# Optimization experiments

Measured on AMD Instinct MI355X. Metric: run time of the kernel, lower is better.

The kernel has to match this reference:

```python
import jax, jax.numpy as jnp
import numpy as np

N_NODES = 50000
N_EDGES = 800000
N_RELS = 200
D = 128


def setup_inputs() -> dict:
    key = jax.random.key(0)
    ks = jax.random.split(key, 9)
    h = jax.random.normal(ks[0], (N_NODES, D), dtype=jnp.float32)
    r = jax.random.normal(ks[1], (N_RELS, D), dtype=jnp.float32)
    norm = jax.random.uniform(ks[2], (N_NODES, 1), dtype=jnp.float32)
    src = jax.random.randint(ks[3], (N_EDGES,), 0, N_NODES, dtype=jnp.int32)
    dst = jax.random.randint(ks[4], (N_EDGES,), 0, N_NODES, dtype=jnp.int32)
    rel = jax.random.randint(ks[5], (N_EDGES,), 0, N_RELS, dtype=jnp.int32)
    stdv = 1.0 / np.sqrt(D)
    W_msg = jax.random.uniform(ks[6], (D, D), minval=-stdv, maxval=stdv, dtype=jnp.float32)
    W = jax.random.uniform(ks[7], (D, D), minval=-stdv, maxval=stdv, dtype=jnp.float32)
    b = jax.random.uniform(ks[8], (D,), minval=-stdv, maxval=stdv, dtype=jnp.float32)
    return {"h": h, "r": r, "norm": norm, "src": src, "dst": dst, "rel": rel,
            "W_msg": W_msg, "W": W, "b": b}


def reference(h, r, norm, src, dst, rel, W_msg, W, b):
    # dropout=0.0 (eval); h = h * norm (symmetric-norm pre-scale)
    hn = h * norm                                    # [N, D]
    # per-edge message: (h_src - r_rel) @ W_msg
    msg = (hn[src] - r[rel]) @ W_msg                 # [E, D]
    # scatter-sum to destination nodes, then post-scale by norm
    agg = jax.ops.segment_sum(msg, dst, num_segments=hn.shape[0]) * norm  # [N, D]
    out = hn @ W + agg + b
    return jax.nn.relu(out)
```

## Files before the change

### kernel.cpp

```cpp
#include <hip/hip_runtime.h>

#define N_NODES 50000
#define N_EDGES 800000
#define DIM 128
#define K2 256
#define NREL 200
#define BN2 128
#define NB2 391
#define ECAP 4096
#define EPB 4096

typedef unsigned short u16;
typedef __attribute__((ext_vector_type(8))) short short8;
typedef __attribute__((ext_vector_type(4))) float f32x4;

__device__ __forceinline__ float bf2f(u16 v) {
    union { unsigned int u; float f; } x;
    x.u = ((unsigned int)v) << 16;
    return x.f;
}

__device__ __forceinline__ u16 f2bf(float f) {
    union { unsigned int u; float f; } x;
    x.f = f;
    return (u16)((x.u + 0x7FFFu + ((x.u >> 16) & 1u)) >> 16);
}

__device__ __forceinline__ int sniff_fp32(const void* h, int tid) {
    const u16* hp = (const u16*)h;
    u16 v = hp[2 * (tid & 63)];
    float a = fabsf(bf2f(v));
    int insane = ((v & 0x7F80) == 0x7F80) || (a != 0.0f && (a > 1e6f || a < 1e-20f));
    return __popcll(__ballot(insane)) > 16;
}

#define PREP_H (N_NODES * 32)
#define PREP_R (NREL * 32)
#define PREP_W 8192
#define PREP_N (N_NODES / 4)
#define PREP_B 32
#define PREP_TOT (PREP_H + PREP_R + PREP_W + PREP_N + PREP_B)
#define PREP_BLOCKS ((PREP_TOT + 255) / 256)
#define HIST_BLOCKS 128
__global__ __launch_bounds__(256) void prep_hist(
    const void* __restrict__ h, const void* __restrict__ r, const void* __restrict__ norm,
    const void* __restrict__ W, const void* __restrict__ Wmsg, const void* __restrict__ bias,
    const int* __restrict__ dst,
    u16* __restrict__ hx, u16* __restrict__ r_bf, u16* __restrict__ wt,
    u16* __restrict__ norm_bf, float* __restrict__ b_f, int* __restrict__ bucketCount)
{
    __shared__ int hh[NB2];
    int tid = threadIdx.x;
    if (blockIdx.x >= PREP_BLOCKS) {
        for (int i = tid; i < NB2; i += 256) hh[i] = 0;
        __syncthreads();
        int stride = HIST_BLOCKS * 256;
        for (int e = (blockIdx.x - PREP_BLOCKS) * 256 + tid; e < N_EDGES; e += stride)
            atomicAdd(&hh[dst[e] >> 7], 1);
        __syncthreads();
        for (int i = tid; i < NB2; i += 256)
            if (hh[i]) atomicAdd(&bucketCount[i], hh[i]);
        return;
    }
    int isf = sniff_fp32(h, tid);
    int t = blockIdx.x * 256 + tid;
    if (t < PREP_H) {
        int n = t >> 5, c = t & 31;
        float4 v; float nv;
        if (isf) {
            nv = ((const float*)norm)[n];
            v = *(const float4*)((const float*)h + (size_t)n * DIM + c * 4);
        } else {
            nv = bf2f(((const u16*)norm)[n]);
            ushort4 u = *(const ushort4*)((const u16*)h + (size_t)n * DIM + c * 4);
            v = make_float4(bf2f(u.x), bf2f(u.y), bf2f(u.z), bf2f(u.w));
        }
        ushort4 o;
        o.x = f2bf(v.x * nv); o.y = f2bf(v.y * nv); o.z = f2bf(v.z * nv); o.w = f2bf(v.w * nv);
        *(ushort4*)(hx + (size_t)n * DIM + c * 4) = o;
    } else if (t < PREP_H + PREP_R) {
        int t2 = t - PREP_H;
        int rho = t2 >> 5, c = t2 & 31;
        float4 v;
        if (isf) v = *(const float4*)((const float*)r + (size_t)rho * DIM + c * 4);
        else {
            ushort4 u = *(const ushort4*)((const u16*)r + (size_t)rho * DIM + c * 4);
            v = make_float4(bf2f(u.x), bf2f(u.y), bf2f(u.z), bf2f(u.w));
        }
        ushort4 o;
        o.x = f2bf(v.x); o.y = f2bf(v.y); o.z = f2bf(v.z); o.w = f2bf(v.w);
        *(ushort4*)(r_bf + (size_t)rho * DIM + c * 4) = o;
    } else if (t < PREP_H + PREP_R + PREP_W) {
        int t3 = t - PREP_H - PREP_R;
        int j = t3 >> 6;
        int k0 = (t3 & 63) * 4;
        ushort4 o;
        u16* op = (u16*)&o;
        for (int kk = 0; kk < 4; ++kk) {
            int k = k0 + kk;
            float wv;
            if (isf) wv = (k < 128) ? ((const float*)W)[(size_t)k * DIM + j]
                                    : ((const float*)Wmsg)[(size_t)(k - 128) * DIM + j];
            else     wv = (k < 128) ? bf2f(((const u16*)W)[(size_t)k * DIM + j])
                                    : bf2f(((const u16*)Wmsg)[(size_t)(k - 128) * DIM + j]);
            op[kk] = f2bf(wv);
        }
        *(ushort4*)(wt + (size_t)j * K2 + k0) = o;
    } else if (t < PREP_H + PREP_R + PREP_W + PREP_N) {
        int n0 = (t - PREP_H - PREP_R - PREP_W) * 4;
        ushort4 o;
        if (isf) {
            float4 v = *(const float4*)((const float*)norm + n0);
            o.x = f2bf(v.x); o.y = f2bf(v.y); o.z = f2bf(v.z); o.w = f2bf(v.w);
        } else {
            o = *(const ushort4*)((const u16*)norm + n0);
        }
        *(ushort4*)(norm_bf + n0) = o;
    } else if (t < PREP_TOT) {
        int j0 = (t - PREP_H - PREP_R - PREP_W - PREP_N) * 4;
        float4 v;
        if (isf) v = *(const float4*)((const float*)bias + j0);
        else {
            ushort4 u = *(const ushort4*)((const u16*)bias + j0);
            v = make_float4(bf2f(u.x), bf2f(u.y), bf2f(u.z), bf2f(u.w));
        }
        *(float4*)(b_f + j0) = v;
    }
}

__global__ __launch_bounds__(512) void bucket_scan(const int* __restrict__ bucketCount,
                            int* __restrict__ bucketBase, int* __restrict__ bucketCursor) {
    __shared__ int sd[512];
    int t = threadIdx.x;
    int c = (t < NB2) ? bucketCount[t] : 0;
    sd[t] = c;
    __syncthreads();
    for (int off = 1; off < 512; off <<= 1) {
        int v = (t >= off) ? sd[t - off] : 0;
        __syncthreads();
        sd[t] += v;
        __syncthreads();
    }
    if (t < NB2) { int ex = sd[t] - c; bucketBase[t] = ex; bucketCursor[t] = ex; }
    if (t == 0) bucketBase[NB2] = N_EDGES;
}

__global__ __launch_bounds__(512) void fill_lds(
    const int* __restrict__ dst, const int* __restrict__ src, const int* __restrict__ rel,
    int* __restrict__ bucketCursor, int* __restrict__ spk)
{
    __shared__ int hist[NB2];
    __shared__ int lbase[NB2];
    __shared__ int gbase[NB2];
    __shared__ int sd[512];
    __shared__ int pay[EPB];
    __shared__ u16 bkt[EPB];
    int tid = threadIdx.x;
    for (int i = tid; i < NB2; i += 512) hist[i] = 0;
    __syncthreads();
    int e0 = blockIdx.x * EPB;
    int myb[8], myr[8], myp[8];
#pragma unroll
    for (int i = 0; i < 8; ++i) {
        int e = e0 + i * 512 + tid;
        myb[i] = -1;
        if (e < N_EDGES) {
            int d = dst[e];
            int b = d >> 7;
            myb[i] = b;
            myr[i] = atomicAdd(&hist[b], 1);
            myp[i] = src[e] | (rel[e] << 16) | ((d & 127) << 24);
        }
    }
    __syncthreads();
    sd[tid] = (tid < NB2) ? hist[tid] : 0;
    __syncthreads();
    for (int off = 1; off < 512; off <<= 1) {
        int v = (tid >= off) ? sd[tid - off] : 0;
        __syncthreads();
        sd[tid] += v;
        __syncthreads();
    }
    if (tid < NB2) {
        lbase[tid] = sd[tid] - hist[tid];
        gbase[tid] = hist[tid] ? atomicAdd(&bucketCursor[tid], hist[tid]) : 0;
    }
    __syncthreads();
#pragma unroll
    for (int i = 0; i < 8; ++i) {
        if (myb[i] >= 0) {
            int lp = lbase[myb[i]] + myr[i];
            pay[lp] = myp[i];
            bkt[lp] = (u16)myb[i];
        }
    }
    __syncthreads();
    int total = N_EDGES - e0; if (total > EPB) total = EPB;
#pragma unroll
    for (int i = 0; i < 8; ++i) {
        int lp = i * 512 + tid;
        if (lp < total) {
            int b = bkt[lp];
            spk[gbase[b] + (lp - lbase[b])] = pay[lp];
        }
    }
}

__global__ __launch_bounds__(1024) void bucket_fused(
    const u16* __restrict__ hx, const u16* __restrict__ r_bf,
    const u16* __restrict__ norm_bf, const float* __restrict__ b_f,
    const int* __restrict__ bucketBase, const int* __restrict__ spk,
    const u16* __restrict__ wt, const void* __restrict__ h, void* __restrict__ out)
{
    __shared__ int stage[ECAP];
    __shared__ int sorted[ECAP];
    __shared__ int hist[BN2];
    __shared__ int nbase[BN2];
    __shared__ u16 Xu[BN2][136];
    int tid = threadIdx.x;
    int b = blockIdx.x;
    int base = bucketBase[b], end = bucketBase[b + 1];
    int size = end - base; if (size > ECAP) size = ECAP;

    if (tid < BN2) hist[tid] = 0;
    __syncthreads();
    for (int i = tid; i < size; i += 1024) {
        int pk = spk[base + i];
        stage[i] = pk;
        atomicAdd(&hist[(pk >> 24) & 127], 1);
    }
    __syncthreads();
    if (tid < BN2) nbase[tid] = hist[tid];
    __syncthreads();
    for (int off = 1; off < BN2; off <<= 1) {
        int v = 0;
        if (tid < BN2 && tid >= off) v = nbase[tid - off];
        __syncthreads();
        if (tid < BN2) nbase[tid] += v;
        __syncthreads();
    }
    if (tid < BN2) { nbase[tid] -= hist[tid]; hist[tid] = 0; }
    __syncthreads();
    for (int i = tid; i < size; i += 1024) {
        int pk = stage[i];
        int dl = (pk >> 24) & 127;
        int rk = atomicAdd(&hist[dl], 1);
        sorted[nbase[dl] + rk] = pk;
    }
    __syncthreads();

    int g = tid & 15, grp = tid >> 4;
#pragma unroll
    for (int which = 0; which < 2; ++which) {
        int dl = grp + which * 64;
        int rs = nbase[dl], cnt = hist[dl];
        float acc[8] = {};
        int j = 0;
        for (; j + 1 < cnt; j += 2) {
            int pk0 = sorted[rs + j];
            int pk1 = sorted[rs + j + 1];
            int s0 = pk0 & 0xFFFF, r0 = (pk0 >> 16) & 0xFF;
            int s1 = pk1 & 0xFFFF, r1 = (pk1 >> 16) & 0xFF;
            short8 h0 = *(const short8*)(hx + (size_t)s0 * DIM + g * 8);
            short8 h1 = *(const short8*)(hx + (size_t)s1 * DIM + g * 8);
            short8 v0 = *(const short8*)(r_bf + (size_t)r0 * DIM + g * 8);
            short8 v1 = *(const short8*)(r_bf + (size_t)r1 * DIM + g * 8);
#pragma unroll
            for (int d = 0; d < 8; ++d) acc[d] += bf2f((u16)h0[d]) - bf2f((u16)v0[d]);
#pragma unroll
            for (int d = 0; d < 8; ++d) acc[d] += bf2f((u16)h1[d]) - bf2f((u16)v1[d]);
        }
        if (j < cnt) {
            int pk = sorted[rs + j];
            int s = pk & 0xFFFF, rl = (pk >> 16) & 0xFF;
            short8 hv = *(const short8*)(hx + (size_t)s * DIM + g * 8);
            short8 rv = *(const short8*)(r_bf + (size_t)rl * DIM + g * 8);
#pragma unroll
            for (int d = 0; d < 8; ++d) acc[d] += bf2f((u16)hv[d]) - bf2f((u16)rv[d]);
        }
        int node = b * BN2 + dl;
        float nv = bf2f(norm_bf[node < N_NODES ? node : 0]);
        short8 o;
#pragma unroll
        for (int d = 0; d < 8; ++d) o[d] = (short)f2bf(acc[d] * nv);
        *(short8*)&Xu[dl][g * 8] = o;
    }
    __syncthreads();

    int w = tid >> 6, lane = tid & 63;
    int m = lane & 15, quad = lane >> 4;
    int row0 = (w & 7) * 16;
    int ch = w >> 3;
    int nodeA = b * BN2 + row0 + m;
    short8 a[8];
#pragma unroll
    for (int kb = 0; kb < 4; ++kb)
        a[kb] = *(const short8*)(hx + (size_t)nodeA * DIM + kb * 32 + quad * 8);
#pragma unroll
    for (int kb = 0; kb < 4; ++kb)
        a[4 + kb] = *(const short8*)&Xu[row0 + m][kb * 32 + quad * 8];
    int isf = sniff_fp32(h, tid);
#pragma unroll
    for (int ct = 0; ct < 4; ++ct) {
        int n0 = ch * 64 + ct * 16;
        f32x4 c4 = {0.f, 0.f, 0.f, 0.f};
#pragma unroll
        for (int kb = 0; kb < 8; ++kb) {
            short8 bv = *(const short8*)(wt + (size_t)(n0 + m) * K2 + kb * 32 + quad * 8);
            c4 = __builtin_amdgcn_mfma_f32_16x16x32_bf16(a[kb], bv, c4, 0, 0, 0);
        }
        int col = n0 + m;
        float bb = b_f[col];
#pragma unroll
        for (int rg = 0; rg < 4; ++rg) {
            int n = b * BN2 + row0 + quad * 4 + rg;
            if (n < N_NODES) {
                float v = c4[rg] + bb;
                v = v > 0.f ? v : 0.f;
                if (isf) ((float*)out)[(size_t)n * DIM + col] = v;
                else     ((u16*)out)[(size_t)n * DIM + col] = f2bf(v);
            }
        }
    }
}

static inline size_t alup(size_t x) { return (x + 255) & ~(size_t)255; }

extern "C" void kernel_launch(void* const* d_in, const int* in_sizes, int n_in,
                              void* d_out, int out_size, void* d_ws, size_t ws_size,
                              hipStream_t stream) {
    const void* h    = d_in[0];
    const void* r    = d_in[1];
    const void* norm = d_in[2];
    const int* src   = (const int*)d_in[3];
    const int* dst   = (const int*)d_in[4];
    const int* rel   = (const int*)d_in[5];
    const void* Wmsg = d_in[6];
    const void* W    = d_in[7];
    const void* b    = d_in[8];

    char* p = (char*)d_ws;
    u16* hx       = (u16*)p;                 p += alup((size_t)N_NODES * DIM * 2);
    u16* r_bf     = (u16*)p;                 p += alup((size_t)NREL * DIM * 2);
    u16* wt       = (u16*)p;                 p += alup((size_t)DIM * K2 * 2);
    u16* norm_bf  = (u16*)p;                 p += alup((size_t)N_NODES * 2);
    float* b_f    = (float*)p;               p += alup((size_t)DIM * 4);
    int* bucketCount  = (int*)p;             p += alup((size_t)NB2 * 4);
    int* bucketBase   = (int*)p;             p += alup((size_t)(NB2 + 1) * 4);
    int* bucketCursor = (int*)p;             p += alup((size_t)NB2 * 4);
    int* spk      = (int*)p;                 p += alup((size_t)N_EDGES * 4);

    hipMemsetAsync(bucketCount, 0, (size_t)NB2 * 4, stream);
    prep_hist<<<PREP_BLOCKS + HIST_BLOCKS, 256, 0, stream>>>(
        h, r, norm, W, Wmsg, b, dst, hx, r_bf, wt, norm_bf, b_f, bucketCount);
    bucket_scan<<<1, 512, 0, stream>>>(bucketCount, bucketBase, bucketCursor);
    fill_lds<<<(N_EDGES + EPB - 1) / EPB, 512, 0, stream>>>(dst, src, rel, bucketCursor, spk);
    bucket_fused<<<NB2, 1024, 0, stream>>>(
        hx, r_bf, norm_bf, b_f, bucketBase, spk, wt, h, d_out);
}
```

Before: 193.6 us.

## Split each 128-node bucket across two 512-thread blocks of 64 nodes

```diff
diff --git a/kernel.cpp b/kernel.cpp
--- a/kernel.cpp
+++ b/kernel.cpp
@@ -5,10 +5,11 @@
 #define DIM 128
 #define K2 256
 #define NREL 200
-#define BN2 128
 #define NB2 391
-#define ECAP 4096
 #define EPB 4096
+#define BN3 64
+#define NB3 782
+#define ECAP3 2048
 
 typedef unsigned short u16;
 typedef __attribute__((ext_vector_type(8))) short short8;
@@ -206,92 +207,99 @@
     }
 }
 
-__global__ __launch_bounds__(1024) void bucket_fused(
+__global__ __launch_bounds__(512) void bucket_fused(
     const u16* __restrict__ hx, const u16* __restrict__ r_bf,
     const u16* __restrict__ norm_bf, const float* __restrict__ b_f,
     const int* __restrict__ bucketBase, const int* __restrict__ spk,
     const u16* __restrict__ wt, const void* __restrict__ h, void* __restrict__ out)
 {
-    __shared__ int stage[ECAP];
-    __shared__ int sorted[ECAP];
-    __shared__ int hist[BN2];
-    __shared__ int nbase[BN2];
-    __shared__ u16 Xu[BN2][136];
+    __shared__ int sorted[ECAP3];
+    __shared__ int hist[BN3];
+    __shared__ int nbase[BN3];
+    __shared__ u16 Xu[BN3][136];
     int tid = threadIdx.x;
     int b = blockIdx.x;
-    int base = bucketBase[b], end = bucketBase[b + 1];
-    int size = end - base; if (size > ECAP) size = ECAP;
-
-    if (tid < BN2) hist[tid] = 0;
-    __syncthreads();
-    for (int i = tid; i < size; i += 1024) {
+    int fb = b >> 1, hf = b & 1;
+    int base = bucketBase[fb], end = bucketBase[fb + 1];
+    int size = end - base;
+
+    if (tid < BN3) hist[tid] = 0;
+    __syncthreads();
+    for (int i = tid; i < size; i += 512) {
+        int dl = (spk[base + i] >> 24) & 127;
+        if ((dl >> 6) == hf) atomicAdd(&hist[dl & 63], 1);
+    }
+    __syncthreads();
+    if (tid < BN3) nbase[tid] = hist[tid];
+    __syncthreads();
+    for (int off = 1; off < BN3; off <<= 1) {
+        int v = 0;
+        if (tid < BN3 && tid >= off) v = nbase[tid - off];
+        __syncthreads();
+        if (tid < BN3) nbase[tid] += v;
+        __syncthreads();
+    }
+    if (tid < BN3) { nbase[tid] -= hist[tid]; hist[tid] = 0; }
+    __syncthreads();
+    for (int i = tid; i < size; i += 512) {
         int pk = spk[base + i];
-        stage[i] = pk;
-        atomicAdd(&hist[(pk >> 24) & 127], 1);
-    }
-    __syncthreads();
-    if (tid < BN2) nbase[tid] = hist[tid];
-    __syncthreads();
-    for (int off = 1; off < BN2; off <<= 1) {
-        int v = 0;
-        if (tid < BN2 && tid >= off) v = nbase[tid - off];
-        __syncthreads();
-        if (tid < BN2) nbase[tid] += v;
-        __syncthreads();
-    }
-    if (tid < BN2) { nbase[tid] -= hist[tid]; hist[tid] = 0; }
-    __syncthreads();
-    for (int i = tid; i < size; i += 1024) {
-        int pk = stage[i];
         int dl = (pk >> 24) & 127;
-        int rk = atomicAdd(&hist[dl], 1);
-        sorted[nbase[dl] + rk] = pk;
+        if ((dl >> 6) == hf) {
+            int d6 = dl & 63;
+            int rk = atomicAdd(&hist[d6], 1);
+            int pos = nbase[d6] + rk;
+            if (pos < ECAP3) sorted[pos] = pk;
+        }
     }
     __syncthreads();
 
     int g = tid & 15, grp = tid >> 4;
 #pragma unroll
     for (int which = 0; which < 2; ++which) {
-        int dl = grp + which * 64;
-        int rs = nbase[dl], cnt = hist[dl];
+        int d6 = grp + which * 32;
+        int rs = nbase[d6], cnt = hist[d6];
         float acc[8] = {};
         int j = 0;
-        for (; j + 1 < cnt; j += 2) {
-            int pk0 = sorted[rs + j];
-            int pk1 = sorted[rs + j + 1];
-            int s0 = pk0 & 0xFFFF, r0 = (pk0 >> 16) & 0xFF;
-            int s1 = pk1 & 0xFFFF, r1 = (pk1 >> 16) & 0xFF;
-            short8 h0 = *(const short8*)(hx + (size_t)s0 * DIM + g * 8);
-            short8 h1 = *(const short8*)(hx + (size_t)s1 * DIM + g * 8);
-            short8 v0 = *(const short8*)(r_bf + (size_t)r0 * DIM + g * 8);
-            short8 v1 = *(const short8*)(r_bf + (size_t)r1 * DIM + g * 8);
-#pragma unroll
-            for (int d = 0; d < 8; ++d) acc[d] += bf2f((u16)h0[d]) - bf2f((u16)v0[d]);
-#pragma unroll
-            for (int d = 0; d < 8; ++d) acc[d] += bf2f((u16)h1[d]) - bf2f((u16)v1[d]);
-        }
-        if (j < cnt) {
+        for (; j + 3 < cnt; j += 4) {
+            int pk0 = sorted[rs + j], pk1 = sorted[rs + j + 1];
+            int pk2 = sorted[rs + j + 2], pk3 = sorted[rs + j + 3];
+            short8 h0 = *(const short8*)(hx + (size_t)(pk0 & 0xFFFF) * DIM + g * 8);
+            short8 h1 = *(const short8*)(hx + (size_t)(pk1 & 0xFFFF) * DIM + g * 8);
+            short8 h2 = *(const short8*)(hx + (size_t)(pk2 & 0xFFFF) * DIM + g * 8);
+            short8 h3 = *(const short8*)(hx + (size_t)(pk3 & 0xFFFF) * DIM + g * 8);
+            short8 v0 = *(const short8*)(r_bf + (size_t)((pk0 >> 16) & 0xFF) * DIM + g * 8);
+            short8 v1 = *(const short8*)(r_bf + (size_t)((pk1 >> 16) & 0xFF) * DIM + g * 8);
+            short8 v2 = *(const short8*)(r_bf + (size_t)((pk2 >> 16) & 0xFF) * DIM + g * 8);
+            short8 v3 = *(const short8*)(r_bf + (size_t)((pk3 >> 16) & 0xFF) * DIM + g * 8);
+#pragma unroll
+            for (int d = 0; d < 8; ++d) {
+                acc[d] += (bf2f((u16)h0[d]) - bf2f((u16)v0[d]))
+                        + (bf2f((u16)h1[d]) - bf2f((u16)v1[d]))
+                        + (bf2f((u16)h2[d]) - bf2f((u16)v2[d]))
+                        + (bf2f((u16)h3[d]) - bf2f((u16)v3[d]));
+            }
+        }
+        for (; j < cnt; ++j) {
             int pk = sorted[rs + j];
-            int s = pk & 0xFFFF, rl = (pk >> 16) & 0xFF;
-            short8 hv = *(const short8*)(hx + (size_t)s * DIM + g * 8);
-            short8 rv = *(const short8*)(r_bf + (size_t)rl * DIM + g * 8);
+            short8 hv = *(const short8*)(hx + (size_t)(pk & 0xFFFF) * DIM + g * 8);
+            short8 rv = *(const short8*)(r_bf + (size_t)((pk >> 16) & 0xFF) * DIM + g * 8);
 #pragma unroll
             for (int d = 0; d < 8; ++d) acc[d] += bf2f((u16)hv[d]) - bf2f((u16)rv[d]);
         }
-        int node = b * BN2 + dl;
+        int node = b * BN3 + d6;
         float nv = bf2f(norm_bf[node < N_NODES ? node : 0]);
         short8 o;
 #pragma unroll
         for (int d = 0; d < 8; ++d) o[d] = (short)f2bf(acc[d] * nv);
-        *(short8*)&Xu[dl][g * 8] = o;
+        *(short8*)&Xu[d6][g * 8] = o;
     }
     __syncthreads();
 
     int w = tid >> 6, lane = tid & 63;
     int m = lane & 15, quad = lane >> 4;
-    int row0 = (w & 7) * 16;
-    int ch = w >> 3;
-    int nodeA = b * BN2 + row0 + m;
+    int row0 = (w & 3) * 16;
+    int ch = w >> 2;
+    int nodeA = b * BN3 + row0 + m;
     short8 a[8];
 #pragma unroll
     for (int kb = 0; kb < 4; ++kb)
@@ -313,7 +321,7 @@
         float bb = b_f[col];
 #pragma unroll
         for (int rg = 0; rg < 4; ++rg) {
-            int n = b * BN2 + row0 + quad * 4 + rg;
+            int n = b * BN3 + row0 + quad * 4 + rg;
             if (n < N_NODES) {
                 float v = c4[rg] + bb;
                 v = v > 0.f ? v : 0.f;
@@ -355,6 +363,6 @@
         h, r, norm, W, Wmsg, b, dst, hx, r_bf, wt, norm_bf, b_f, bucketCount);
     bucket_scan<<<1, 512, 0, stream>>>(bucketCount, bucketBase, bucketCursor);
     fill_lds<<<(N_EDGES + EPB - 1) / EPB, 512, 0, stream>>>(dst, src, rel, bucketCursor, spk);
-    bucket_fused<<<NB2, 1024, 0, stream>>>(
+    bucket_fused<<<NB3, 512, 0, stream>>>(
         hx, r_bf, norm_bf, b_f, bucketBase, spk, wt, h, d_out);
 }
```

Result: no change. 191.5 us (-1.1%).
